# Kernel tuning notes

Measured on AMD Instinct MI355X. Metric: run time of the kernel, lower is better.

The kernel has to match this reference:

```python
import jax, jax.numpy as jnp
import numpy as np

B, T, E = 2048, 200, 128
H1, H2 = 64, 32
NEG_INF = -(2.0 ** 32) + 1.0  # matches tf source's -2**32 + 1 padding value


def setup_inputs() -> dict:
    key = jax.random.key(0)
    ks = jax.random.split(key, 8)
    queries = jax.random.normal(ks[0], (B, E), dtype=jnp.float32)
    keys = jax.random.normal(ks[1], (B, T, E), dtype=jnp.float32)
    keys_id = jax.random.randint(ks[2], (B, T), 0, 2, dtype=jnp.int32)
    # Dense params: MLP input is concat([q,k,q-k,q*k]) -> 4*E = 512
    W1 = jax.random.normal(ks[3], (4 * E, H1), dtype=jnp.float32) * (1.0 / np.sqrt(4 * E))
    b1 = jnp.zeros((H1,), dtype=jnp.float32)
    W2 = jax.random.normal(ks[4], (H1, H2), dtype=jnp.float32) * (1.0 / np.sqrt(H1))
    b2 = jnp.zeros((H2,), dtype=jnp.float32)
    W3 = jax.random.normal(ks[5], (H2, 1), dtype=jnp.float32) * (1.0 / np.sqrt(H2))
    b3 = jnp.zeros((1,), dtype=jnp.float32)
    return {"queries": queries, "keys": keys, "keys_id": keys_id,
            "W1": W1, "b1": b1, "W2": W2, "b2": b2, "W3": W3, "b3": b3}


def reference(queries, keys, keys_id, W1, b1, W2, b2, W3, b3):
    # tile query over the time axis: [B,E] -> [B,T,E]
    q = jnp.broadcast_to(queries[:, None, :], keys.shape)
    # concat features: [B,T,4E]
    feat = jnp.concatenate([q, keys, q - keys, q * keys], axis=2)
    # small MLP scorer
    h = jax.nn.relu(jnp.einsum('btf,fh->bth', feat, W1) + b1)
    h = jax.nn.relu(jnp.einsum('bth,hk->btk', h, W2) + b2)
    weight = jnp.einsum('btk,ko->bto', h, W3) + b3  # [B,T,1]
    # masked softmax over time axis (padding id == 0)
    mask = (keys_id != 0)[:, :, None]  # [B,T,1]
    weight = jnp.where(mask, weight, jnp.float32(NEG_INF))
    weight = jax.nn.softmax(weight, axis=1)
    # weighted mean pooling (original uses reduce_mean, i.e. sum/T)
    return jnp.mean(weight * keys, axis=1)  # [B,E]
```

## Files before the change

kernel.cpp:

```cpp
#include <hip/hip_runtime.h>

#define NEG_INF_F (-4294967295.0f)

typedef __attribute__((ext_vector_type(8))) short bf16x8;
typedef __attribute__((ext_vector_type(4))) float f32x4;

__device__ __forceinline__ unsigned short f2bf(float x) {
    unsigned u = __float_as_uint(x);
    unsigned r = (u + 0x7fffu + ((u >> 16) & 1u)) >> 16;
    return (unsigned short)r;
}
__device__ __forceinline__ float bf2f(unsigned short s) {
    return __uint_as_float(((unsigned)s) << 16);
}

struct __align__(16) Smem {
    unsigned short K[200 * 128];
    unsigned short h1s[4][16 * 64];
    float q[128];
    float maskf[208];
    float cpart[256];
    float s[208];
    float ppart[128];
    float red[16];
};
static_assert(sizeof(Smem) <= 64 * 1024, "LDS over 64 KiB");

__global__ __launch_bounds__(256, 2)
void attn_fused(const float* __restrict__ Q,
                const float* __restrict__ Kg,
                const int*   __restrict__ kid,
                const float* __restrict__ W1,
                const float* __restrict__ b1,
                const float* __restrict__ W2,
                const float* __restrict__ b2,
                const float* __restrict__ W3,
                const float* __restrict__ b3,
                float* __restrict__ out)
{
    __shared__ Smem sm;
    const int b    = blockIdx.x;
    const int tid  = threadIdx.x;
    const int wave = tid >> 6;
    const int lane = tid & 63;
    const int l15  = lane & 15;
    const int quad = lane >> 4;

    if (tid < 128) sm.q[tid] = Q[b * 128 + tid];
    if (tid < 200) sm.maskf[tid] = (kid[b * 200 + tid] != 0) ? 1.0f : 0.0f;
    __syncthreads();

    {
        const int n = tid & 63, kc = tid >> 6;
        float acc = (kc == 0) ? b1[n] : 0.0f;
        #pragma unroll 4
        for (int i = 0; i < 32; ++i) {
            const int k = kc * 32 + i;
            acc += sm.q[k] * (W1[k * 64 + n] + W1[(256 + k) * 64 + n]);
        }
        sm.cpart[kc * 64 + n] = acc;
    }

    {
        const float4* src = reinterpret_cast<const float4*>(Kg + (size_t)b * 200 * 128);
        #pragma unroll
        for (int r = 0; r < 25; ++r) {
            const int idx4 = tid + 256 * r;
            const float4 v = src[idx4];
            const int t = idx4 >> 5;
            const int e = (idx4 & 31) << 2;
            const int g = (e >> 3) ^ (t & 15);
            ushort4 pk;
            pk.x = f2bf(v.x); pk.y = f2bf(v.y); pk.z = f2bf(v.z); pk.w = f2bf(v.w);
            *reinterpret_cast<ushort4*>(&sm.K[t * 128 + g * 8 + (e & 7)]) = pk;
        }
    }
    __syncthreads();

    bf16x8 Mf[4][4];
    #pragma unroll
    for (int ks = 0; ks < 4; ++ks) {
        #pragma unroll
        for (int nt = 0; nt < 4; ++nt) {
            const int n = nt * 16 + l15;
            const int kb = ks * 32 + quad * 8;
            bf16x8 f;
            #pragma unroll
            for (int j = 0; j < 8; ++j) {
                const int k = kb + j;
                const float wb = W1[(128 + k) * 64 + n];
                const float wd = W1[(256 + k) * 64 + n];
                const float wp = W1[(384 + k) * 64 + n];
                f[j] = (short)f2bf((wb - wd) + sm.q[k] * wp);
            }
            Mf[ks][nt] = f;
        }
    }
    bf16x8 W2f[2][2];
    #pragma unroll
    for (int ks = 0; ks < 2; ++ks) {
        #pragma unroll
        for (int nt = 0; nt < 2; ++nt) {
            const int n = nt * 16 + l15;
            const int kb = ks * 32 + quad * 8;
            bf16x8 f;
            #pragma unroll
            for (int j = 0; j < 8; ++j) f[j] = (short)f2bf(W2[(kb + j) * 32 + n]);
            W2f[ks][nt] = f;
        }
    }
    const float w3a = W3[l15],  w3b = W3[16 + l15];
    const float b2a = b2[l15],  b2b = b2[16 + l15];
    const float b3v = b3[0];
    float cn[4];
    #pragma unroll
    for (int nt = 0; nt < 4; ++nt) {
        const int n = nt * 16 + l15;
        cn[nt] = sm.cpart[n] + sm.cpart[64 + n] + sm.cpart[128 + n] + sm.cpart[192 + n];
    }

    unsigned short* h1w = &sm.h1s[wave][0];
    const f32x4 zero4 = {0.f, 0.f, 0.f, 0.f};

    for (int tile = wave; tile < 13; tile += 4) {
        const int t0 = tile * 16;
        const int t  = t0 + l15;
        f32x4 acc[4] = {zero4, zero4, zero4, zero4};
        #pragma unroll
        for (int ks = 0; ks < 4; ++ks) {
            const int g = (ks * 4 + quad) ^ (t & 15);
            const bf16x8 A = *reinterpret_cast<const bf16x8*>(&sm.K[t * 128 + g * 8]);
            #pragma unroll
            for (int nt = 0; nt < 4; ++nt)
                acc[nt] = __builtin_amdgcn_mfma_f32_16x16x32_bf16(A, Mf[ks][nt], acc[nt], 0, 0, 0);
        }
        #pragma unroll
        for (int nt = 0; nt < 4; ++nt) {
            const int n = nt * 16 + l15;
            #pragma unroll
            for (int r = 0; r < 4; ++r) {
                const int m = quad * 4 + r;
                const float h = fmaxf(acc[nt][r] + cn[nt], 0.0f);
                const int g = (n >> 3) ^ (m & 7);
                h1w[m * 64 + g * 8 + (n & 7)] = f2bf(h);
            }
        }
        f32x4 p0 = zero4, p1 = zero4;
        #pragma unroll
        for (int ks = 0; ks < 2; ++ks) {
            const int g = (ks * 4 + quad) ^ (l15 & 7);
            const bf16x8 A2 = *reinterpret_cast<const bf16x8*>(&h1w[l15 * 64 + g * 8]);
            p0 = __builtin_amdgcn_mfma_f32_16x16x32_bf16(A2, W2f[ks][0], p0, 0, 0, 0);
            p1 = __builtin_amdgcn_mfma_f32_16x16x32_bf16(A2, W2f[ks][1], p1, 0, 0, 0);
        }
        float sv[4];
        #pragma unroll
        for (int r = 0; r < 4; ++r)
            sv[r] = fmaxf(p0[r] + b2a, 0.f) * w3a + fmaxf(p1[r] + b2b, 0.f) * w3b;
        #pragma unroll
        for (int off = 1; off < 16; off <<= 1) {
            #pragma unroll
            for (int r = 0; r < 4; ++r) sv[r] += __shfl_xor(sv[r], off);
        }
        if (l15 == 0) {
            #pragma unroll
            for (int r = 0; r < 4; ++r) {
                const int tt = t0 + quad * 4 + r;
                if (tt < 200)
                    sm.s[tt] = (sm.maskf[tt] != 0.0f) ? (sv[r] + b3v) : NEG_INF_F;
                else if (tt < 208)
                    sm.s[tt] = -__builtin_inff();
            }
        }
    }
    __syncthreads();

    {
        const float v = (tid < 208) ? sm.s[tid] : -__builtin_inff();
        float m = v;
        #pragma unroll
        for (int off = 32; off >= 1; off >>= 1) m = fmaxf(m, __shfl_xor(m, off));
        if (lane == 0) sm.red[wave] = m;
        __syncthreads();
        m = fmaxf(fmaxf(sm.red[0], sm.red[1]), fmaxf(sm.red[2], sm.red[3]));
        const float ev = (tid < 208) ? __expf(v - m) : 0.0f;
        float ssum = ev;
        #pragma unroll
        for (int off = 32; off >= 1; off >>= 1) ssum += __shfl_xor(ssum, off);
        if (lane == 0) sm.red[8 + wave] = ssum;
        __syncthreads();
        const float S = sm.red[8] + sm.red[9] + sm.red[10] + sm.red[11];
        const float inv = 1.0f / (S * 200.0f);
        if (tid < 208) sm.s[tid] = ev * inv;
    }
    __syncthreads();

    {
        const int e = tid & 127;
        const int h = tid >> 7;
        float acc2 = 0.0f;
        const int tbeg = h * 100;
        for (int tt = tbeg; tt < tbeg + 100; ++tt) {
            const float wv = sm.s[tt];
            const int g = (e >> 3) ^ (tt & 15);
            acc2 += wv * bf2f(sm.K[tt * 128 + g * 8 + (e & 7)]);
        }
        if (h == 1) sm.ppart[e] = acc2;
        __syncthreads();
        if (h == 0) out[(size_t)b * 128 + e] = acc2 + sm.ppart[e];
    }
}

extern "C" void kernel_launch(void* const* d_in, const int* in_sizes, int n_in,
                              void* d_out, int out_size, void* d_ws, size_t ws_size,
                              hipStream_t stream) {
    (void)in_sizes; (void)n_in; (void)out_size; (void)d_ws; (void)ws_size;
    attn_fused<<<dim3(2048), dim3(256), 0, stream>>>(
        (const float*)d_in[0], (const float*)d_in[1], (const int*)d_in[2],
        (const float*)d_in[3], (const float*)d_in[4], (const float*)d_in[5],
        (const float*)d_in[6], (const float*)d_in[7], (const float*)d_in[8],
        (float*)d_out);
}
```

Measured before the change: 354.0 us.

## Cooperatively build W1 fragments via LDS, issue K loads first, unroll pooling

Each wave previously built its own W1-derived MFMA fragments with redundant strided global loads. That work is now split across all threads, staged through LDS in two halves and read back as fragments. The K tile load is moved ahead of the other setup so its latency overlaps with it, and float-to-bf16 conversion uses a paired intrinsic. The pooling loop is fully unrolled with four accumulators and vectorized weight reads. The change adds extra barriers and reuses the h1 scratch buffer, and the four accumulators change summation order slightly.

```diff
diff --git a/kernel.cpp b/kernel.cpp
--- a/kernel.cpp
+++ b/kernel.cpp
@@ -1,4 +1,5 @@
 #include <hip/hip_runtime.h>
+#include <hip/hip_bf16.h>
 
 #define NEG_INF_F (-4294967295.0f)
 
@@ -7,8 +8,11 @@
 
 __device__ __forceinline__ unsigned short f2bf(float x) {
     unsigned u = __float_as_uint(x);
-    unsigned r = (u + 0x7fffu + ((u >> 16) & 1u)) >> 16;
-    return (unsigned short)r;
+    return (unsigned short)((u + 0x7fffu + ((u >> 16) & 1u)) >> 16);
+}
+__device__ __forceinline__ unsigned f2bf2(float a, float b) {
+    __hip_bfloat162 h2 = __float22bfloat162_rn(make_float2(a, b));
+    unsigned r; __builtin_memcpy(&r, &h2, 4); return r;
 }
 __device__ __forceinline__ float bf2f(unsigned short s) {
     return __uint_as_float(((unsigned)s) << 16);
@@ -46,9 +50,41 @@
     const int l15  = lane & 15;
     const int quad = lane >> 4;
 
+    {
+        const float4* src = reinterpret_cast<const float4*>(Kg + (size_t)b * 200 * 128);
+        #pragma unroll
+        for (int r = 0; r < 25; ++r) {
+            const int idx4 = tid + 256 * r;
+            const float4 v = src[idx4];
+            const int t = idx4 >> 5;
+            const int e = (idx4 & 31) << 2;
+            const int g = (e >> 3) ^ (t & 15);
+            uint2 pk;
+            pk.x = f2bf2(v.x, v.y);
+            pk.y = f2bf2(v.z, v.w);
+            *reinterpret_cast<uint2*>(&sm.K[t * 128 + g * 8 + (e & 7)]) = pk;
+        }
+    }
     if (tid < 128) sm.q[tid] = Q[b * 128 + tid];
     if (tid < 200) sm.maskf[tid] = (kid[b * 200 + tid] != 0) ? 1.0f : 0.0f;
     __syncthreads();
+
+    bf16x8 W2f[2][2];
+    #pragma unroll
+    for (int ks = 0; ks < 2; ++ks) {
+        #pragma unroll
+        for (int nt = 0; nt < 2; ++nt) {
+            const int n = nt * 16 + l15;
+            const int kb = ks * 32 + quad * 8;
+            bf16x8 f;
+            #pragma unroll
+            for (int j = 0; j < 8; ++j) f[j] = (short)f2bf(W2[(kb + j) * 32 + n]);
+            W2f[ks][nt] = f;
+        }
+    }
+    const float w3a = W3[l15],  w3b = W3[16 + l15];
+    const float b2a = b2[l15],  b2b = b2[16 + l15];
+    const float b3v = b3[0];
 
     {
         const int n = tid & 63, kc = tid >> 6;
@@ -61,57 +97,37 @@
         sm.cpart[kc * 64 + n] = acc;
     }
 
-    {
-        const float4* src = reinterpret_cast<const float4*>(Kg + (size_t)b * 200 * 128);
-        #pragma unroll
-        for (int r = 0; r < 25; ++r) {
-            const int idx4 = tid + 256 * r;
-            const float4 v = src[idx4];
-            const int t = idx4 >> 5;
-            const int e = (idx4 & 31) << 2;
-            const int g = (e >> 3) ^ (t & 15);
-            ushort4 pk;
-            pk.x = f2bf(v.x); pk.y = f2bf(v.y); pk.z = f2bf(v.z); pk.w = f2bf(v.w);
-            *reinterpret_cast<ushort4*>(&sm.K[t * 128 + g * 8 + (e & 7)]) = pk;
-        }
-    }
-    __syncthreads();
-
     bf16x8 Mf[4][4];
-    #pragma unroll
-    for (int ks = 0; ks < 4; ++ks) {
-        #pragma unroll
-        for (int nt = 0; nt < 4; ++nt) {
-            const int n = nt * 16 + l15;
-            const int kb = ks * 32 + quad * 8;
-            bf16x8 f;
-            #pragma unroll
-            for (int j = 0; j < 8; ++j) {
-                const int k = kb + j;
-                const float wb = W1[(128 + k) * 64 + n];
-                const float wd = W1[(256 + k) * 64 + n];
-                const float wp = W1[(384 + k) * 64 + n];
-                f[j] = (short)f2bf((wb - wd) + sm.q[k] * wp);
-            }
-            Mf[ks][nt] = f;
-        }
-    }
-    bf16x8 W2f[2][2];
-    #pragma unroll
-    for (int ks = 0; ks < 2; ++ks) {
-        #pragma unroll
-        for (int nt = 0; nt < 2; ++nt) {
-            const int n = nt * 16 + l15;
-            const int kb = ks * 32 + quad * 8;
-            bf16x8 f;
-            #pragma unroll
-            for (int j = 0; j < 8; ++j) f[j] = (short)f2bf(W2[(kb + j) * 32 + n]);
-            W2f[ks][nt] = f;
-        }
-    }
-    const float w3a = W3[l15],  w3b = W3[16 + l15];
-    const float b2a = b2[l15],  b2b = b2[16 + l15];
-    const float b3v = b3[0];
+    {
+        unsigned short* Mbuf = &sm.h1s[0][0];
+        const int n   = tid & 63;
+        const int w16 = (tid >> 6) * 16;
+        #pragma unroll
+        for (int hf = 0; hf < 2; ++hf) {
+            #pragma unroll
+            for (int j = 0; j < 16; j += 2) {
+                const int kp = w16 + j;
+                const int k  = hf * 64 + kp;
+                const float v0 = (W1[(128 + k) * 64 + n] - W1[(256 + k) * 64 + n])
+                               + sm.q[k] * W1[(384 + k) * 64 + n];
+                const float v1 = (W1[(129 + k) * 64 + n] - W1[(257 + k) * 64 + n])
+                               + sm.q[k + 1] * W1[(385 + k) * 64 + n];
+                const int g = (kp >> 3) ^ (n & 7);
+                *reinterpret_cast<unsigned*>(&Mbuf[n * 64 + g * 8 + (kp & 7)]) = f2bf2(v0, v1);
+            }
+            __syncthreads();
+            #pragma unroll
+            for (int ksl = 0; ksl < 2; ++ksl) {
+                #pragma unroll
+                for (int nt = 0; nt < 4; ++nt) {
+                    const int nn = nt * 16 + l15;
+                    const int g  = (ksl * 4 + quad) ^ (nn & 7);
+                    Mf[hf * 2 + ksl][nt] = *reinterpret_cast<const bf16x8*>(&Mbuf[nn * 64 + g * 8]);
+                }
+            }
+            __syncthreads();
+        }
+    }
     float cn[4];
     #pragma unroll
     for (int nt = 0; nt < 4; ++nt) {
@@ -196,15 +212,22 @@
     __syncthreads();
 
     {
-        const int e = tid & 127;
-        const int h = tid >> 7;
-        float acc2 = 0.0f;
-        const int tbeg = h * 100;
-        for (int tt = tbeg; tt < tbeg + 100; ++tt) {
-            const float wv = sm.s[tt];
-            const int g = (e >> 3) ^ (tt & 15);
-            acc2 += wv * bf2f(sm.K[tt * 128 + g * 8 + (e & 7)]);
-        }
+        const int e  = tid & 127;
+        const int h  = tid >> 7;
+        const int e3 = e & 7;
+        const int eh = e >> 3;
+        float a0 = 0.f, a1 = 0.f, a2 = 0.f, a3 = 0.f;
+        const int tb0 = h * 100;
+        #pragma unroll
+        for (int i = 0; i < 25; ++i) {
+            const int tb = tb0 + i * 4;
+            const float4 wv = *reinterpret_cast<const float4*>(&sm.s[tb]);
+            a0 += wv.x * bf2f(sm.K[(tb + 0) * 128 + ((eh ^ ((tb + 0) & 15)) * 8) + e3]);
+            a1 += wv.y * bf2f(sm.K[(tb + 1) * 128 + ((eh ^ ((tb + 1) & 15)) * 8) + e3]);
+            a2 += wv.z * bf2f(sm.K[(tb + 2) * 128 + ((eh ^ ((tb + 2) & 15)) * 8) + e3]);
+            a3 += wv.w * bf2f(sm.K[(tb + 3) * 128 + ((eh ^ ((tb + 3) & 15)) * 8) + e3]);
+        }
+        const float acc2 = (a0 + a1) + (a2 + a3);
         if (h == 1) sm.ppart[e] = acc2;
         __syncthreads();
         if (h == 0) out[(size_t)b * 128 + e] = acc2 + sm.ppart[e];
```

New measurement: 345.8 us. -2.3%, faster.

## Stream keys from registers with online softmax instead of staging K in LDS

Applied to the files above, without the earlier changes.

The full bf16 K tile is no longer staged in LDS. Each wave loads its key rows straight into registers, converts them for the MFMA A operand, and keeps an online (flash-style) softmax with a running weighted sum O in registers. The per-wave partials are merged at the end. The precomputed W1 combination is moved from per-lane register fragments into a swizzled LDS matrix, which shrinks LDS use and lets launch bounds rise to 3 blocks per CU. This removes the separate softmax and pooling passes and the LDS traffic for K, and pooling now uses fp32 keys. The cost is more registers (32 O values plus the key loads), a shuffle reduction of 32 values per wave, and B fragments read from LDS inside the MFMA loop.

```diff
diff --git a/kernel.cpp b/kernel.cpp
--- a/kernel.cpp
+++ b/kernel.cpp
@@ -1,4 +1,5 @@
 #include <hip/hip_runtime.h>
+#include <hip/hip_bf16.h>
 
 #define NEG_INF_F (-4294967295.0f)
 
@@ -7,26 +8,24 @@
 
 __device__ __forceinline__ unsigned short f2bf(float x) {
     unsigned u = __float_as_uint(x);
-    unsigned r = (u + 0x7fffu + ((u >> 16) & 1u)) >> 16;
-    return (unsigned short)r;
-}
-__device__ __forceinline__ float bf2f(unsigned short s) {
-    return __uint_as_float(((unsigned)s) << 16);
-}
+    return (unsigned short)((u + 0x7fffu + ((u >> 16) & 1u)) >> 16);
+}
+__device__ __forceinline__ unsigned f2bf2(float a, float b) {
+    __hip_bfloat162 h2 = __float22bfloat162_rn(make_float2(a, b));
+    unsigned r; __builtin_memcpy(&r, &h2, 4); return r;
+}
+union FragU { unsigned u[4]; bf16x8 h; };
 
 struct __align__(16) Smem {
-    unsigned short K[200 * 128];
+    unsigned short Mt[64 * 128];
     unsigned short h1s[4][16 * 64];
     float q[128];
-    float maskf[208];
     float cpart[256];
-    float s[208];
-    float ppart[128];
-    float red[16];
+    float Om[4][128];
+    float mw[4], lw[4];
 };
-static_assert(sizeof(Smem) <= 64 * 1024, "LDS over 64 KiB");
-
-__global__ __launch_bounds__(256, 2)
+
+__global__ __launch_bounds__(256, 3)
 void attn_fused(const float* __restrict__ Q,
                 const float* __restrict__ Kg,
                 const int*   __restrict__ kid,
@@ -47,9 +46,39 @@
     const int quad = lane >> 4;
 
     if (tid < 128) sm.q[tid] = Q[b * 128 + tid];
-    if (tid < 200) sm.maskf[tid] = (kid[b * 200 + tid] != 0) ? 1.0f : 0.0f;
+
+    bf16x8 W2f[2][2];
+    #pragma unroll
+    for (int ks = 0; ks < 2; ++ks) {
+        #pragma unroll
+        for (int nt = 0; nt < 2; ++nt) {
+            const int n = nt * 16 + l15;
+            const int kb = ks * 32 + quad * 8;
+            bf16x8 f;
+            #pragma unroll
+            for (int j = 0; j < 8; ++j) f[j] = (short)f2bf(W2[(kb + j) * 32 + n]);
+            W2f[ks][nt] = f;
+        }
+    }
+    const float w3a = W3[l15],  w3b = W3[16 + l15];
+    const float b2a = b2[l15],  b2b = b2[16 + l15];
+    const float b3v = b3[0];
     __syncthreads();
 
+    {
+        const int n  = tid & 63;
+        const int ko = (tid >> 6) * 2;
+        #pragma unroll
+        for (int i = 0; i < 16; ++i) {
+            const int k = i * 8 + ko;
+            const float v0 = (W1[(128 + k) * 64 + n] - W1[(256 + k) * 64 + n])
+                           + sm.q[k] * W1[(384 + k) * 64 + n];
+            const float v1 = (W1[(129 + k) * 64 + n] - W1[(257 + k) * 64 + n])
+                           + sm.q[k + 1] * W1[(385 + k) * 64 + n];
+            const int g = (k >> 3) ^ (n & 15);
+            *reinterpret_cast<unsigned*>(&sm.Mt[n * 128 + g * 8 + (k & 7)]) = f2bf2(v0, v1);
+        }
+    }
     {
         const int n = tid & 63, kc = tid >> 6;
         float acc = (kc == 0) ? b1[n] : 0.0f;
@@ -60,58 +89,8 @@
         }
         sm.cpart[kc * 64 + n] = acc;
     }
-
-    {
-        const float4* src = reinterpret_cast<const float4*>(Kg + (size_t)b * 200 * 128);
-        #pragma unroll
-        for (int r = 0; r < 25; ++r) {
-            const int idx4 = tid + 256 * r;
-            const float4 v = src[idx4];
-            const int t = idx4 >> 5;
-            const int e = (idx4 & 31) << 2;
-            const int g = (e >> 3) ^ (t & 15);
-            ushort4 pk;
-            pk.x = f2bf(v.x); pk.y = f2bf(v.y); pk.z = f2bf(v.z); pk.w = f2bf(v.w);
-            *reinterpret_cast<ushort4*>(&sm.K[t * 128 + g * 8 + (e & 7)]) = pk;
-        }
-    }
     __syncthreads();
 
-    bf16x8 Mf[4][4];
-    #pragma unroll
-    for (int ks = 0; ks < 4; ++ks) {
-        #pragma unroll
-        for (int nt = 0; nt < 4; ++nt) {
-            const int n = nt * 16 + l15;
-            const int kb = ks * 32 + quad * 8;
-            bf16x8 f;
-            #pragma unroll
-            for (int j = 0; j < 8; ++j) {
-                const int k = kb + j;
-                const float wb = W1[(128 + k) * 64 + n];
-                const float wd = W1[(256 + k) * 64 + n];
-                const float wp = W1[(384 + k) * 64 + n];
-                f[j] = (short)f2bf((wb - wd) + sm.q[k] * wp);
-            }
-            Mf[ks][nt] = f;
-        }
-    }
-    bf16x8 W2f[2][2];
-    #pragma unroll
-    for (int ks = 0; ks < 2; ++ks) {
-        #pragma unroll
-        for (int nt = 0; nt < 2; ++nt) {
-            const int n = nt * 16 + l15;
-            const int kb = ks * 32 + quad * 8;
-            bf16x8 f;
-            #pragma unroll
-            for (int j = 0; j < 8; ++j) f[j] = (short)f2bf(W2[(kb + j) * 32 + n]);
-            W2f[ks][nt] = f;
-        }
-    }
-    const float w3a = W3[l15],  w3b = W3[16 + l15];
-    const float b2a = b2[l15],  b2b = b2[16 + l15];
-    const float b3v = b3[0];
     float cn[4];
     #pragma unroll
     for (int nt = 0; nt < 4; ++nt) {
@@ -119,20 +98,43 @@
         cn[nt] = sm.cpart[n] + sm.cpart[64 + n] + sm.cpart[128 + n] + sm.cpart[192 + n];
     }
 
+    const float* kbase = Kg + (size_t)b * 25600;
     unsigned short* h1w = &sm.h1s[wave][0];
     const f32x4 zero4 = {0.f, 0.f, 0.f, 0.f};
+
+    float O[32];
+    #pragma unroll
+    for (int i = 0; i < 32; ++i) O[i] = 0.0f;
+    float mrun = -__builtin_inff(), lrun = 0.0f;
 
     for (int tile = wave; tile < 13; tile += 4) {
         const int t0 = tile * 16;
         const int t  = t0 + l15;
+        const int tr = min(t, 199);
+        const float* kr = kbase + tr * 128;
+        float4 ka[4], kb_[4];
+        #pragma unroll
+        for (int ks = 0; ks < 4; ++ks) {
+            ka[ks]  = *reinterpret_cast<const float4*>(kr + ks * 32 + quad * 8);
+            kb_[ks] = *reinterpret_cast<const float4*>(kr + ks * 32 + quad * 8 + 4);
+        }
+        const int kidv = kid[b * 200 + tr];
+
         f32x4 acc[4] = {zero4, zero4, zero4, zero4};
         #pragma unroll
         for (int ks = 0; ks < 4; ++ks) {
-            const int g = (ks * 4 + quad) ^ (t & 15);
-            const bf16x8 A = *reinterpret_cast<const bf16x8*>(&sm.K[t * 128 + g * 8]);
-            #pragma unroll
-            for (int nt = 0; nt < 4; ++nt)
-                acc[nt] = __builtin_amdgcn_mfma_f32_16x16x32_bf16(A, Mf[ks][nt], acc[nt], 0, 0, 0);
+            FragU A;
+            A.u[0] = f2bf2(ka[ks].x,  ka[ks].y);
+            A.u[1] = f2bf2(ka[ks].z,  ka[ks].w);
+            A.u[2] = f2bf2(kb_[ks].x, kb_[ks].y);
+            A.u[3] = f2bf2(kb_[ks].z, kb_[ks].w);
+            #pragma unroll
+            for (int nt = 0; nt < 4; ++nt) {
+                const int n = nt * 16 + l15;
+                const int g = (ks * 4 + quad) ^ l15;
+                const bf16x8 Bf = *reinterpret_cast<const bf16x8*>(&sm.Mt[n * 128 + g * 8]);
+                acc[nt] = __builtin_amdgcn_mfma_f32_16x16x32_bf16(A.h, Bf, acc[nt], 0, 0, 0);
+            }
         }
         #pragma unroll
         for (int nt = 0; nt < 4; ++nt) {
@@ -149,9 +151,9 @@
         #pragma unroll
         for (int ks = 0; ks < 2; ++ks) {
             const int g = (ks * 4 + quad) ^ (l15 & 7);
-            const bf16x8 A2 = *reinterpret_cast<const bf16x8*>(&h1w[l15 * 64 + g * 8]);
-            p0 = __builtin_amdgcn_mfma_f32_16x16x32_bf16(A2, W2f[ks][0], p0, 0, 0, 0);
-            p1 = __builtin_amdgcn_mfma_f32_16x16x32_bf16(A2, W2f[ks][1], p1, 0, 0, 0);
+            const bf16x8 A2l = *reinterpret_cast<const bf16x8*>(&h1w[l15 * 64 + g * 8]);
+            p0 = __builtin_amdgcn_mfma_f32_16x16x32_bf16(A2l, W2f[ks][0], p0, 0, 0, 0);
+            p1 = __builtin_amdgcn_mfma_f32_16x16x32_bf16(A2l, W2f[ks][1], p1, 0, 0, 0);
         }
         float sv[4];
         #pragma unroll
@@ -162,52 +164,65 @@
             #pragma unroll
             for (int r = 0; r < 4; ++r) sv[r] += __shfl_xor(sv[r], off);
         }
-        if (l15 == 0) {
-            #pragma unroll
-            for (int r = 0; r < 4; ++r) {
-                const int tt = t0 + quad * 4 + r;
-                if (tt < 200)
-                    sm.s[tt] = (sm.maskf[tt] != 0.0f) ? (sv[r] + b3v) : NEG_INF_F;
-                else if (tt < 208)
-                    sm.s[tt] = -__builtin_inff();
-            }
-        }
-    }
+        const int src = (l15 >> 2) * 16;
+        const float s0 = __shfl(sv[0], src), s1 = __shfl(sv[1], src);
+        const float s2 = __shfl(sv[2], src), s3 = __shfl(sv[3], src);
+        const int rr = l15 & 3;
+        const float sres = (rr == 0) ? s0 : (rr == 1) ? s1 : (rr == 2) ? s2 : s3;
+        float x;
+        if (t < 200) x = (kidv != 0) ? (sres + b3v) : NEG_INF_F;
+        else         x = -__builtin_inff();
+        float tmax = x;
+        #pragma unroll
+        for (int off = 1; off < 16; off <<= 1) tmax = fmaxf(tmax, __shfl_xor(tmax, off));
+        const float mnew  = fmaxf(mrun, tmax);
+        const float alpha = __expf(mrun - mnew);
+        const float w     = __expf(x - mnew);
+        float tsum = w;
+        #pragma unroll
+        for (int off = 1; off < 16; off <<= 1) tsum += __shfl_xor(tsum, off);
+        lrun = lrun * alpha + tsum;
+        mrun = mnew;
+        #pragma unroll
+        for (int ks = 0; ks < 4; ++ks) {
+            O[ks*8+0] = fmaf(O[ks*8+0], alpha, w * ka[ks].x);
+            O[ks*8+1] = fmaf(O[ks*8+1], alpha, w * ka[ks].y);
+            O[ks*8+2] = fmaf(O[ks*8+2], alpha, w * ka[ks].z);
+            O[ks*8+3] = fmaf(O[ks*8+3], alpha, w * ka[ks].w);
+            O[ks*8+4] = fmaf(O[ks*8+4], alpha, w * kb_[ks].x);
+            O[ks*8+5] = fmaf(O[ks*8+5], alpha, w * kb_[ks].y);
+            O[ks*8+6] = fmaf(O[ks*8+6], alpha, w * kb_[ks].z);
+            O[ks*8+7] = fmaf(O[ks*8+7], alpha, w * kb_[ks].w);
+        }
+    }
+
+    #pragma unroll
+    for (int off = 1; off < 16; off <<= 1) {
+        #pragma unroll
+        for (int i = 0; i < 32; ++i) O[i] += __shfl_xor(O[i], off);
+    }
+    if (l15 == 0) {
+        #pragma unroll
+        for (int ks = 0; ks < 4; ++ks) {
+            *reinterpret_cast<float4*>(&sm.Om[wave][ks * 32 + quad * 8]) =
+                make_float4(O[ks*8+0], O[ks*8+1], O[ks*8+2], O[ks*8+3]);
+            *reinterpret_cast<float4*>(&sm.Om[wave][ks * 32 + quad * 8 + 4]) =
+                make_float4(O[ks*8+4], O[ks*8+5], O[ks*8+6], O[ks*8+7]);
+        }
+    }
+    if (lane == 0) { sm.mw[wave] = mrun; sm.lw[wave] = lrun; }
     __syncthreads();
 
-    {
-        const float v = (tid < 208) ? sm.s[tid] : -__builtin_inff();
-        float m = v;
-        #pragma unroll
-        for (int off = 32; off >= 1; off >>= 1) m = fmaxf(m, __shfl_xor(m, off));
-        if (lane == 0) sm.red[wave] = m;
-        __syncthreads();
-        m = fmaxf(fmaxf(sm.red[0], sm.red[1]), fmaxf(sm.red[2], sm.red[3]));
-        const float ev = (tid < 208) ? __expf(v - m) : 0.0f;
-        float ssum = ev;
-        #pragma unroll
-        for (int off = 32; off >= 1; off >>= 1) ssum += __shfl_xor(ssum, off);
-        if (lane == 0) sm.red[8 + wave] = ssum;
-        __syncthreads();
-        const float S = sm.red[8] + sm.red[9] + sm.red[10] + sm.red[11];
-        const float inv = 1.0f / (S * 200.0f);
-        if (tid < 208) sm.s[tid] = ev * inv;
-    }
-    __syncthreads();
-
-    {
-        const int e = tid & 127;
-        const int h = tid >> 7;
-        float acc2 = 0.0f;
-        const int tbeg = h * 100;
-        for (int tt = tbeg; tt < tbeg + 100; ++tt) {
-            const float wv = sm.s[tt];
-            const int g = (e >> 3) ^ (tt & 15);
-            acc2 += wv * bf2f(sm.K[tt * 128 + g * 8 + (e & 7)]);
-        }
-        if (h == 1) sm.ppart[e] = acc2;
-        __syncthreads();
-        if (h == 0) out[(size_t)b * 128 + e] = acc2 + sm.ppart[e];
+    if (tid < 128) {
+        const float M = fmaxf(fmaxf(sm.mw[0], sm.mw[1]), fmaxf(sm.mw[2], sm.mw[3]));
+        float den = 0.f, val = 0.f;
+        #pragma unroll
+        for (int w = 0; w < 4; ++w) {
+            const float a = __expf(sm.mw[w] - M);
+            den += sm.lw[w] * a;
+            val += sm.Om[w][tid] * a;
+        }
+        out[(size_t)b * 128 + tid] = val / (den * 200.0f);
     }
 }
 
```

Result: faster. 325.7 us (-8.0%).
